# Optimization experiments

Measured on AMD Instinct MI355X. Metric: run time of the kernel, lower is better.

## Reference

```python
import jax, jax.numpy as jnp
import numpy as np

N_NODES = 100000
N_EDGES = 800000
F_DIM = 64
N_GRAPHS = 64


def _gcn_layer(h, W, b, src, dst, dis):
    # h: [N, F]; symmetric-normalized GCN conv with self-loops (PyG GCNConv semantics)
    hw = h @ W                                   # dense projection [N, F]
    norm = dis[src] * dis[dst]                   # [E]
    agg = jax.ops.segment_sum(hw[src] * norm[:, None], dst, num_segments=N_NODES)
    agg = agg + (dis * dis)[:, None] * hw        # self-loop contribution
    return agg + b


def setup_inputs() -> dict:
    key = jax.random.key(0)
    ks = jax.random.split(key, 10)
    x = jax.random.normal(ks[0], (N_NODES, F_DIM), dtype=jnp.float32)
    edge_index = jax.random.randint(ks[1], (2, N_EDGES), 0, N_NODES, dtype=jnp.int64 if jax.config.jax_enable_x64 else jnp.int32)
    batch = jnp.sort(jax.random.randint(ks[2], (N_NODES,), 0, N_GRAPHS, dtype=jnp.int32))
    scale = 1.0 / np.sqrt(F_DIM)
    W1 = jax.random.normal(ks[3], (F_DIM, F_DIM), dtype=jnp.float32) * scale
    b1 = jnp.zeros((F_DIM,), dtype=jnp.float32)
    W2 = jax.random.normal(ks[4], (F_DIM, F_DIM), dtype=jnp.float32) * scale
    b2 = jnp.zeros((F_DIM,), dtype=jnp.float32)
    W3 = jax.random.normal(ks[5], (F_DIM, F_DIM), dtype=jnp.float32) * scale
    b3 = jnp.zeros((F_DIM,), dtype=jnp.float32)
    return {"x": x, "edge_index": edge_index, "batch": batch,
            "W1": W1, "b1": b1, "W2": W2, "b2": b2, "W3": W3, "b3": b3}


def reference(x, edge_index, batch, W1, b1, W2, b2, W3, b3):
    src, dst = edge_index[0], edge_index[1]
    # degree with self-loops: deg[i] = 1 + in-degree(i)
    deg = jax.ops.segment_sum(jnp.ones((N_EDGES,), dtype=x.dtype), dst, num_segments=N_NODES) + 1.0
    dis = jax.lax.rsqrt(deg)                     # deg >= 1 always
    h = jax.nn.relu(_gcn_layer(x, W1, b1, src, dst, dis))
    h = jax.nn.relu(_gcn_layer(h, W2, b2, src, dst, dis))
    h = _gcn_layer(h, W3, b3, src, dst, dis)
    # global max pool over graphs in the batch
    out = jax.ops.segment_max(h, batch, num_segments=N_GRAPHS)
    return out
```

## Files before the change

kernel.cpp:

```cpp
#include <hip/hip_runtime.h>
#include <math.h>

#define N_NODES  100000
#define N_EDGES  800000
#define F        64
#define N_GRAPHS 64
#define NQUADS   25000
#define ROWB     128
#define COLCAP   3500000
#define SENT     (N_NODES * ROWB)

typedef _Float16 half8 __attribute__((ext_vector_type(8)));
typedef float    f32x4 __attribute__((ext_vector_type(4)));

#define OFF_BUFA 0u
#define OFF_BUFB 12800256u
#define OFF_DIS  25600512u
#define OFF_DEG  26000512u
#define OFF_QB   26400512u
#define OFF_BSUM 26500544u
#define OFF_COL  26501120u
#define OFF_WT   40501120u
#define OFF_RANK 40525696u

__device__ inline ushort f2bf(float f) {
    uint u = __float_as_uint(f);
    u = (u + 0x7FFFu + ((u >> 16) & 1u)) >> 16;
    return (ushort)u;
}
__device__ inline float bf2f(ushort s) {
    return __uint_as_float(((uint)s) << 16);
}

__device__ inline void atomicMaxFloat(float* addr, float v) {
    if (v >= 0.f) atomicMax((int*)addr, __float_as_int(v));
    else          atomicMin((unsigned int*)addr, __float_as_uint(v));
}

__global__ void k_init(const float* __restrict__ W1, const float* __restrict__ W2,
                       const float* __restrict__ W3, _Float16* __restrict__ Wt,
                       ushort* __restrict__ bufA, ushort* __restrict__ bufB,
                       float* __restrict__ out, int* __restrict__ degcnt,
                       int* __restrict__ col) {
    int tid = blockIdx.x * blockDim.x + threadIdx.x;
    int stride = gridDim.x * blockDim.x;
    for (int i = tid; i < COLCAP; i += stride) col[i] = SENT;
    for (int i = tid; i < N_NODES; i += stride) degcnt[i] = 0;
    if (tid < 3 * 4096) {
        int wsel = tid >> 12, i = tid & 4095;
        int k = i >> 6, f = i & 63;
        const float* Ws = (wsel == 0) ? W1 : (wsel == 1) ? W2 : W3;
        Wt[wsel * 4096 + f * 64 + k] = (_Float16)Ws[k * 64 + f];
    } else if (tid < 3 * 4096 + 64) {
        int f = tid - 3 * 4096;
        bufA[(size_t)N_NODES * F + f] = 0;
        bufB[(size_t)N_NODES * F + f] = 0;
    } else if (tid < 3 * 4096 + 64 + N_GRAPHS * F) {
        out[tid - (3 * 4096 + 64)] = -INFINITY;
    }
}

__global__ void k_degree(const int* __restrict__ dst, int* __restrict__ degcnt,
                         int* __restrict__ rank) {
    int e = blockIdx.x * blockDim.x + threadIdx.x;
    if (e < N_EDGES) rank[e] = atomicAdd(&degcnt[dst[e]], 1);
}

__global__ void k_quad(const int* __restrict__ degcnt, int* __restrict__ qbase,
                       int* __restrict__ bsum, float* __restrict__ dis) {
    __shared__ int s[1024];
    int q = blockIdx.x * 1024 + threadIdx.x;
    int tot = 0;
    if (q < NQUADS) {
        const int4 d4 = *(const int4*)(degcnt + q * 4);
        float4 dv;
        dv.x = rsqrtf((float)d4.x + 1.0f);
        dv.y = rsqrtf((float)d4.y + 1.0f);
        dv.z = rsqrtf((float)d4.z + 1.0f);
        dv.w = rsqrtf((float)d4.w + 1.0f);
        *(float4*)(dis + q * 4) = dv;
        int m = max(max(d4.x, d4.y), max(d4.z, d4.w));
        int P = (m + 3) & ~3;
        tot = 4 * P;
    }
    s[threadIdx.x] = tot;
    __syncthreads();
    for (int off = 1; off < 1024; off <<= 1) {
        int t = (threadIdx.x >= off) ? s[threadIdx.x - off] : 0;
        __syncthreads();
        s[threadIdx.x] += t;
        __syncthreads();
    }
    if (q < NQUADS) qbase[q + 1] = s[threadIdx.x];
    if (threadIdx.x == 1023) bsum[blockIdx.x] = s[1023];
}

__global__ void k_scan3px(int* __restrict__ qbase, const int* __restrict__ bsum,
                          const float* __restrict__ x, const float* __restrict__ dis,
                          ushort* __restrict__ xs) {
    if (blockIdx.x < 25) {
        __shared__ int soff;
        if (threadIdx.x == 0) {
            int acc = 0;
            for (int j = 0; j < (int)blockIdx.x; ++j) acc += bsum[j];
            soff = acc;
        }
        __syncthreads();
        int off = soff;
        int q = blockIdx.x * 1024 + threadIdx.x;
        if (q < NQUADS) qbase[q + 1] += off;
        if (q == 0) qbase[0] = 0;
    } else {
        int t = (blockIdx.x - 25) * 1024 + threadIdx.x;
        if (t < N_NODES * 8) {
            int n = t >> 3;
            float d = dis[n];
            const float4* px = (const float4*)(x + (size_t)t * 8);
            float4 a = px[0], b = px[1];
            ushort o[8] = { f2bf(d*a.x), f2bf(d*a.y), f2bf(d*a.z), f2bf(d*a.w),
                            f2bf(d*b.x), f2bf(d*b.y), f2bf(d*b.z), f2bf(d*b.w) };
            *(uint4*)(xs + (size_t)t * 8) = *(const uint4*)o;
        }
    }
}

__global__ void k_fill(const int* __restrict__ src, const int* __restrict__ dst,
                       const int* __restrict__ qbase, const int* __restrict__ rank,
                       int* __restrict__ col) {
    int e = blockIdx.x * blockDim.x + threadIdx.x;
    if (e < N_EDGES) {
        int d = dst[e];
        col[qbase[d >> 2] + rank[e] * 4 + (d & 3)] = src[e] * ROWB;
    }
}

template<bool RELU, bool SCALE, bool POOL>
__global__ __launch_bounds__(256) void k_layer(const ushort* __restrict__ hs,
                                               const int* __restrict__ qbase,
                                               const int* __restrict__ col,
                                               const float* __restrict__ dis,
                                               const _Float16* __restrict__ Wt,
                                               const float* __restrict__ bias,
                                               ushort* __restrict__ hout,
                                               const int* __restrict__ batch,
                                               float* __restrict__ out) {
    __shared__ _Float16 g[64 * 64];
    __shared__ float pl[4 * 64];
    int lane = threadIdx.x & 63;
    int w    = __builtin_amdgcn_readfirstlane(threadIdx.x >> 6);
    int chunk = blockIdx.x * 64;
    int wr16 = w * 16;
    int nbase = chunk + wr16;
    const char* hsb = (const char*)hs;
    int l2 = lane << 1;

    if (POOL) pl[threadIdx.x] = -INFINITY;

    for (int p = 0; p < 4; ++p) {
        int na = nbase + 4 * p;
        int quad = na >> 2;
        int rowb = wr16 + 4 * p;
        bool vq = quad < NQUADS;
        int qb0 = 0, iters = 0;
        if (vq) {
            qb0   = __builtin_amdgcn_readfirstlane(qbase[quad]);
            int qb1 = __builtin_amdgcn_readfirstlane(qbase[quad + 1]);
            iters = (qb1 - qb0) >> 4;
        }
        float a0 = vq ? bf2f(hs[(size_t)(na    ) * F + lane]) : 0.f;
        float a1 = vq ? bf2f(hs[(size_t)(na + 1) * F + lane]) : 0.f;
        float a2 = vq ? bf2f(hs[(size_t)(na + 2) * F + lane]) : 0.f;
        float a3 = vq ? bf2f(hs[(size_t)(na + 3) * F + lane]) : 0.f;
        const int* cp0 = col + qb0;
        for (int i = 0; i < iters; ++i) {
            const int* cp = cp0 + (i << 4);
            float v0  = bf2f(*(const ushort*)(hsb + (uint)cp[0]  + l2));
            float v1  = bf2f(*(const ushort*)(hsb + (uint)cp[1]  + l2));
            float v2  = bf2f(*(const ushort*)(hsb + (uint)cp[2]  + l2));
            float v3  = bf2f(*(const ushort*)(hsb + (uint)cp[3]  + l2));
            float v4  = bf2f(*(const ushort*)(hsb + (uint)cp[4]  + l2));
            float v5  = bf2f(*(const ushort*)(hsb + (uint)cp[5]  + l2));
            float v6  = bf2f(*(const ushort*)(hsb + (uint)cp[6]  + l2));
            float v7  = bf2f(*(const ushort*)(hsb + (uint)cp[7]  + l2));
            float v8  = bf2f(*(const ushort*)(hsb + (uint)cp[8]  + l2));
            float v9  = bf2f(*(const ushort*)(hsb + (uint)cp[9]  + l2));
            float v10 = bf2f(*(const ushort*)(hsb + (uint)cp[10] + l2));
            float v11 = bf2f(*(const ushort*)(hsb + (uint)cp[11] + l2));
            float v12 = bf2f(*(const ushort*)(hsb + (uint)cp[12] + l2));
            float v13 = bf2f(*(const ushort*)(hsb + (uint)cp[13] + l2));
            float v14 = bf2f(*(const ushort*)(hsb + (uint)cp[14] + l2));
            float v15 = bf2f(*(const ushort*)(hsb + (uint)cp[15] + l2));
            a0 += v0 + v4 + v8  + v12;
            a1 += v1 + v5 + v9  + v13;
            a2 += v2 + v6 + v10 + v14;
            a3 += v3 + v7 + v11 + v15;
        }
        float d0 = vq ? dis[na]     : 0.f;
        float d1 = vq ? dis[na + 1] : 0.f;
        float d2 = vq ? dis[na + 2] : 0.f;
        float d3 = vq ? dis[na + 3] : 0.f;
        g[(rowb    ) * 64 + lane] = (_Float16)(d0 * a0);
        g[(rowb + 1) * 64 + lane] = (_Float16)(d1 * a1);
        g[(rowb + 2) * 64 + lane] = (_Float16)(d2 * a2);
        g[(rowb + 3) * 64 + lane] = (_Float16)(d3 * a3);
    }

    int l15 = lane & 15, lh = lane >> 4;
    half8 bfrag[2][4];
#pragma unroll
    for (int ks = 0; ks < 2; ++ks)
#pragma unroll
        for (int nt = 0; nt < 4; ++nt)
            bfrag[ks][nt] = *(const half8*)(Wt + (nt * 16 + l15) * 64 + ks * 32 + lh * 8);

    f32x4 acc4[4] = {};
#pragma unroll
    for (int ks = 0; ks < 2; ++ks) {
        half8 a = *(const half8*)(&g[(wr16 + l15) * 64 + ks * 32 + lh * 8]);
#pragma unroll
        for (int nt = 0; nt < 4; ++nt)
            acc4[nt] = __builtin_amdgcn_mfma_f32_16x16x32_f16(a, bfrag[ks][nt], acc4[nt], 0, 0, 0);
    }

    float bvals[4];
#pragma unroll
    for (int nt = 0; nt < 4; ++nt) bvals[nt] = bias[nt * 16 + l15];

    if (POOL) __syncthreads();
    int gmin = 0;
    if (POOL) gmin = __builtin_amdgcn_readfirstlane(batch[chunk]);

#pragma unroll
    for (int rr = 0; rr < 4; ++rr) {
        int row = wr16 + lh * 4 + rr;
        int ng = chunk + row;
        if (ng < N_NODES) {
            if (POOL) {
                int gb = batch[ng];
                int rel = gb - gmin;
#pragma unroll
                for (int nt = 0; nt < 4; ++nt) {
                    float vv = acc4[nt][rr] + bvals[nt];
                    if (RELU) vv = fmaxf(vv, 0.f);
                    if (rel < 4) atomicMaxFloat(&pl[rel * 64 + nt * 16 + l15], vv);
                    else         atomicMaxFloat(&out[gb * F + nt * 16 + l15], vv);
                }
            } else {
                float ds2 = 1.f;
                if (SCALE) ds2 = dis[ng];
#pragma unroll
                for (int nt = 0; nt < 4; ++nt) {
                    float vv = acc4[nt][rr] + bvals[nt];
                    if (RELU) vv = fmaxf(vv, 0.f);
                    if (SCALE) vv *= ds2;
                    hout[(size_t)ng * F + nt * 16 + l15] = f2bf(vv);
                }
            }
        }
    }
    if (POOL) {
        __syncthreads();
        float v = pl[threadIdx.x];
        int r = threadIdx.x >> 6, c = threadIdx.x & 63;
        int gg = gmin + r;
        if (v != -INFINITY && gg < N_GRAPHS)
            atomicMaxFloat(&out[gg * F + c], v);
    }
}

extern "C" void kernel_launch(void* const* d_in, const int* in_sizes, int n_in,
                              void* d_out, int out_size, void* d_ws, size_t ws_size,
                              hipStream_t stream) {
    const float* x     = (const float*)d_in[0];
    const int*   ei    = (const int*)d_in[1];
    const int*   batch = (const int*)d_in[2];
    const float* W1 = (const float*)d_in[3];
    const float* b1 = (const float*)d_in[4];
    const float* W2 = (const float*)d_in[5];
    const float* b2 = (const float*)d_in[6];
    const float* W3 = (const float*)d_in[7];
    const float* b3 = (const float*)d_in[8];
    const int* src = ei;
    const int* dst = ei + N_EDGES;

    char* ws = (char*)d_ws;
    ushort*   bufA   = (ushort*)(ws + OFF_BUFA);
    ushort*   bufB   = (ushort*)(ws + OFF_BUFB);
    float*    dis    = (float*)(ws + OFF_DIS);
    int*      degcnt = (int*)(ws + OFF_DEG);
    int*      qbase  = (int*)(ws + OFF_QB);
    int*      bsum   = (int*)(ws + OFF_BSUM);
    int*      col    = (int*)(ws + OFF_COL);
    _Float16* wt     = (_Float16*)(ws + OFF_WT);
    int*      rank   = (int*)(ws + OFF_RANK);
    float*    out    = (float*)d_out;

    k_init<<<1024, 256, 0, stream>>>(W1, W2, W3, wt, bufA, bufB, out, degcnt, col);
    k_degree<<<(N_EDGES + 255) / 256, 256, 0, stream>>>(dst, degcnt, rank);
    k_quad<<<25, 1024, 0, stream>>>(degcnt, qbase, bsum, dis);
    k_scan3px<<<25 + (N_NODES * 8 + 1023) / 1024, 1024, 0, stream>>>(qbase, bsum, x, dis, bufA);
    k_fill<<<(N_EDGES + 255) / 256, 256, 0, stream>>>(src, dst, qbase, rank, col);

    const int LBLOCKS = (N_NODES + 63) / 64;
    k_layer<true,  true,  false><<<LBLOCKS, 256, 0, stream>>>(bufA, qbase, col, dis, wt,        b1, bufB, nullptr, nullptr);
    k_layer<true,  true,  false><<<LBLOCKS, 256, 0, stream>>>(bufB, qbase, col, dis, wt + 4096, b2, bufA, nullptr, nullptr);
    k_layer<false, false, true ><<<LBLOCKS, 256, 0, stream>>>(bufA, qbase, col, dis, wt + 8192, b3, bufB, batch, out);
}
```

Measured before the change: 156.6 us.

## Replace prefix-scan CSR offsets with atomic allocation and merge fill kernels

Per-quad column offsets now come from an atomicAdd on a global counter instead of a two-pass block scan, and each quad stores its (base, length) pair. This removes the scan kernel and lets the edge-fill and the x prescale/bf16 conversion run in one launch, cutting launch count and serial dependencies. The cost is that quad segments land in nondeterministic order in col, which can reduce locality of the column reads in the layer kernels. The global atomic is also contended by 25k threads.

```diff
diff --git a/kernel.cpp b/kernel.cpp
--- a/kernel.cpp
+++ b/kernel.cpp
@@ -9,6 +9,7 @@
 #define ROWB     128
 #define COLCAP   3500000
 #define SENT     (N_NODES * ROWB)
+#define FILLB    3125
 
 typedef _Float16 half8 __attribute__((ext_vector_type(8)));
 typedef float    f32x4 __attribute__((ext_vector_type(4)));
@@ -17,11 +18,11 @@
 #define OFF_BUFB 12800256u
 #define OFF_DIS  25600512u
 #define OFF_DEG  26000512u
-#define OFF_QB   26400512u
-#define OFF_BSUM 26500544u
-#define OFF_COL  26501120u
-#define OFF_WT   40501120u
-#define OFF_RANK 40525696u
+#define OFF_QI   26400512u
+#define OFF_TOT  26600576u
+#define OFF_COL  26600640u
+#define OFF_WT   40600640u
+#define OFF_RANK 40625216u
 
 __device__ inline ushort f2bf(float f) {
     uint u = __float_as_uint(f);
@@ -41,11 +42,12 @@
                        const float* __restrict__ W3, _Float16* __restrict__ Wt,
                        ushort* __restrict__ bufA, ushort* __restrict__ bufB,
                        float* __restrict__ out, int* __restrict__ degcnt,
-                       int* __restrict__ col) {
+                       int* __restrict__ col, int* __restrict__ total) {
     int tid = blockIdx.x * blockDim.x + threadIdx.x;
     int stride = gridDim.x * blockDim.x;
     for (int i = tid; i < COLCAP; i += stride) col[i] = SENT;
     for (int i = tid; i < N_NODES; i += stride) degcnt[i] = 0;
+    if (tid == 0) *total = 0;
     if (tid < 3 * 4096) {
         int wsel = tid >> 12, i = tid & 4095;
         int k = i >> 6, f = i & 63;
@@ -66,11 +68,9 @@
     if (e < N_EDGES) rank[e] = atomicAdd(&degcnt[dst[e]], 1);
 }
 
-__global__ void k_quad(const int* __restrict__ degcnt, int* __restrict__ qbase,
-                       int* __restrict__ bsum, float* __restrict__ dis) {
-    __shared__ int s[1024];
-    int q = blockIdx.x * 1024 + threadIdx.x;
-    int tot = 0;
+__global__ void k_quad(const int* __restrict__ degcnt, int* __restrict__ qinfo,
+                       int* __restrict__ total, float* __restrict__ dis) {
+    int q = blockIdx.x * blockDim.x + threadIdx.x;
     if (q < NQUADS) {
         const int4 d4 = *(const int4*)(degcnt + q * 4);
         float4 dv;
@@ -81,37 +81,25 @@
         *(float4*)(dis + q * 4) = dv;
         int m = max(max(d4.x, d4.y), max(d4.z, d4.w));
         int P = (m + 3) & ~3;
-        tot = 4 * P;
-    }
-    s[threadIdx.x] = tot;
-    __syncthreads();
-    for (int off = 1; off < 1024; off <<= 1) {
-        int t = (threadIdx.x >= off) ? s[threadIdx.x - off] : 0;
-        __syncthreads();
-        s[threadIdx.x] += t;
-        __syncthreads();
-    }
-    if (q < NQUADS) qbase[q + 1] = s[threadIdx.x];
-    if (threadIdx.x == 1023) bsum[blockIdx.x] = s[1023];
-}
-
-__global__ void k_scan3px(int* __restrict__ qbase, const int* __restrict__ bsum,
-                          const float* __restrict__ x, const float* __restrict__ dis,
-                          ushort* __restrict__ xs) {
-    if (blockIdx.x < 25) {
-        __shared__ int soff;
-        if (threadIdx.x == 0) {
-            int acc = 0;
-            for (int j = 0; j < (int)blockIdx.x; ++j) acc += bsum[j];
-            soff = acc;
-        }
-        __syncthreads();
-        int off = soff;
-        int q = blockIdx.x * 1024 + threadIdx.x;
-        if (q < NQUADS) qbase[q + 1] += off;
-        if (q == 0) qbase[0] = 0;
+        int tot = 4 * P;
+        int base = atomicAdd(total, tot);
+        qinfo[2 * q]     = base;
+        qinfo[2 * q + 1] = tot;
+    }
+}
+
+__global__ void k_fillpx(const int* __restrict__ src, const int* __restrict__ dst,
+                         const int* __restrict__ qinfo, const int* __restrict__ rank,
+                         int* __restrict__ col, const float* __restrict__ x,
+                         const float* __restrict__ dis, ushort* __restrict__ xs) {
+    if (blockIdx.x < FILLB) {
+        int e = blockIdx.x * 256 + threadIdx.x;
+        if (e < N_EDGES) {
+            int d = dst[e];
+            col[qinfo[2 * (d >> 2)] + rank[e] * 4 + (d & 3)] = src[e] * ROWB;
+        }
     } else {
-        int t = (blockIdx.x - 25) * 1024 + threadIdx.x;
+        int t = (blockIdx.x - FILLB) * 256 + threadIdx.x;
         if (t < N_NODES * 8) {
             int n = t >> 3;
             float d = dis[n];
@@ -124,19 +112,9 @@
     }
 }
 
-__global__ void k_fill(const int* __restrict__ src, const int* __restrict__ dst,
-                       const int* __restrict__ qbase, const int* __restrict__ rank,
-                       int* __restrict__ col) {
-    int e = blockIdx.x * blockDim.x + threadIdx.x;
-    if (e < N_EDGES) {
-        int d = dst[e];
-        col[qbase[d >> 2] + rank[e] * 4 + (d & 3)] = src[e] * ROWB;
-    }
-}
-
 template<bool RELU, bool SCALE, bool POOL>
 __global__ __launch_bounds__(256) void k_layer(const ushort* __restrict__ hs,
-                                               const int* __restrict__ qbase,
+                                               const int* __restrict__ qinfo,
                                                const int* __restrict__ col,
                                                const float* __restrict__ dis,
                                                const _Float16* __restrict__ Wt,
@@ -163,9 +141,8 @@
         bool vq = quad < NQUADS;
         int qb0 = 0, iters = 0;
         if (vq) {
-            qb0   = __builtin_amdgcn_readfirstlane(qbase[quad]);
-            int qb1 = __builtin_amdgcn_readfirstlane(qbase[quad + 1]);
-            iters = (qb1 - qb0) >> 4;
+            qb0   = __builtin_amdgcn_readfirstlane(qinfo[2 * quad]);
+            iters = __builtin_amdgcn_readfirstlane(qinfo[2 * quad + 1]) >> 4;
         }
         float a0 = vq ? bf2f(hs[(size_t)(na    ) * F + lane]) : 0.f;
         float a1 = vq ? bf2f(hs[(size_t)(na + 1) * F + lane]) : 0.f;
@@ -288,21 +265,20 @@
     ushort*   bufB   = (ushort*)(ws + OFF_BUFB);
     float*    dis    = (float*)(ws + OFF_DIS);
     int*      degcnt = (int*)(ws + OFF_DEG);
-    int*      qbase  = (int*)(ws + OFF_QB);
-    int*      bsum   = (int*)(ws + OFF_BSUM);
+    int*      qinfo  = (int*)(ws + OFF_QI);
+    int*      total  = (int*)(ws + OFF_TOT);
     int*      col    = (int*)(ws + OFF_COL);
     _Float16* wt     = (_Float16*)(ws + OFF_WT);
     int*      rank   = (int*)(ws + OFF_RANK);
     float*    out    = (float*)d_out;
 
-    k_init<<<1024, 256, 0, stream>>>(W1, W2, W3, wt, bufA, bufB, out, degcnt, col);
+    k_init<<<1024, 256, 0, stream>>>(W1, W2, W3, wt, bufA, bufB, out, degcnt, col, total);
     k_degree<<<(N_EDGES + 255) / 256, 256, 0, stream>>>(dst, degcnt, rank);
-    k_quad<<<25, 1024, 0, stream>>>(degcnt, qbase, bsum, dis);
-    k_scan3px<<<25 + (N_NODES * 8 + 1023) / 1024, 1024, 0, stream>>>(qbase, bsum, x, dis, bufA);
-    k_fill<<<(N_EDGES + 255) / 256, 256, 0, stream>>>(src, dst, qbase, rank, col);
+    k_quad<<<(NQUADS + 255) / 256, 256, 0, stream>>>(degcnt, qinfo, total, dis);
+    k_fillpx<<<FILLB + (N_NODES * 8 + 255) / 256, 256, 0, stream>>>(src, dst, qinfo, rank, col, x, dis, bufA);
 
     const int LBLOCKS = (N_NODES + 63) / 64;
-    k_layer<true,  true,  false><<<LBLOCKS, 256, 0, stream>>>(bufA, qbase, col, dis, wt,        b1, bufB, nullptr, nullptr);
-    k_layer<true,  true,  false><<<LBLOCKS, 256, 0, stream>>>(bufB, qbase, col, dis, wt + 4096, b2, bufA, nullptr, nullptr);
-    k_layer<false, false, true ><<<LBLOCKS, 256, 0, stream>>>(bufA, qbase, col, dis, wt + 8192, b3, bufB, batch, out);
-}
+    k_layer<true,  true,  false><<<LBLOCKS, 256, 0, stream>>>(bufA, qinfo, col, dis, wt,        b1, bufB, nullptr, nullptr);
+    k_layer<true,  true,  false><<<LBLOCKS, 256, 0, stream>>>(bufB, qinfo, col, dis, wt + 4096, b2, bufA, nullptr, nullptr);
+    k_layer<false, false, true ><<<LBLOCKS, 256, 0, stream>>>(bufA, qinfo, col, dis, wt + 8192, b3, bufB, batch, out);
+}
```

After: 159.3 us. Within noise of the previous version (+1.7%).
